# Kernel optimization log

Hardware: AMD Instinct MI355X
Metric: run time of the kernel (lower is better)

## Reference

```python
import jax, jax.numpy as jnp
import numpy as np

MARGIN = 0.3
NEG_FILL = 1000000.0


def setup_inputs() -> dict:
    key = jax.random.key(0)
    k1, k2 = jax.random.split(key)
    features = jax.random.normal(k1, (8192, 128), dtype=jnp.float32)
    labels = jax.random.randint(k2, (8192,), 0, 512, dtype=jnp.int64)
    return {"features": features, "labels": labels}


def _triplet_loss(features, labels):
    N = features.shape[0]
    # pairwise euclidean distances via gram trick (matches torch.cdist p=2)
    sq = jnp.sum(features * features, axis=1)               # [N]
    d2 = sq[:, None] + sq[None, :] - 2.0 * (features @ features.T)
    d2 = jnp.maximum(d2, 0.0)
    # guard sqrt(0) on diagonal for clean gradients
    dist = jnp.where(d2 > 0.0, jnp.sqrt(jnp.where(d2 > 0.0, d2, 1.0)), 0.0)  # [N,N]

    same = labels[:, None] == labels[None, :]
    eye = jnp.eye(N, dtype=bool)
    is_pos = same & ~eye
    is_neg = ~same

    neg_inf = jnp.float32(-jnp.inf)
    pos_inf = jnp.float32(jnp.inf)
    has_pos = jnp.any(is_pos, axis=1)
    has_neg = jnp.any(is_neg, axis=1)
    # hardest positive: masked row max; empty -> 0.0
    dist_ap = jnp.max(jnp.where(is_pos, dist, neg_inf), axis=1)
    dist_ap = jnp.where(has_pos, dist_ap, 0.0)
    # hardest negative: masked row min; empty -> 1e6
    dist_an = jnp.min(jnp.where(is_neg, dist, pos_inf), axis=1)
    dist_an = jnp.where(has_neg, dist_an, NEG_FILL)

    # MarginRankingLoss with y=1: mean(max(0, margin - (dist_an - dist_ap)))
    return jnp.mean(jnp.maximum(0.0, MARGIN - (dist_an - dist_ap)))


def reference(features, labels):
    return _triplet_loss(features, labels)
```

## Files before the change

### kernel.cpp

```cpp
#include <hip/hip_runtime.h>
#include <hip/hip_bf16.h>
#include <math.h>

#define N 8192
#define D 128
#define MARGIN_V 0.3f
#define NEG_FILL 1000000.0f

typedef short bf16x8 __attribute__((ext_vector_type(8)));
typedef float f32x4  __attribute__((ext_vector_type(4)));


__global__ __launch_bounds__(256) void convert_kernel(const float* __restrict__ F,
                                                      unsigned short* __restrict__ Fb,
                                                      float* __restrict__ sq,
                                                      unsigned* __restrict__ ap,
                                                      unsigned* __restrict__ an) {
    __shared__ float red[16][17];
    const int g   = blockIdx.x;
    const int tid = threadIdx.x;
    const int q = tid >> 6, L = tid & 63;
    const int m = L & 15, j8 = (L >> 4) * 8;

    const float* src = F + (size_t)(16 * g + m) * D + 32 * q + j8;
    float4 v0 = *(const float4*)src;
    float4 v1 = *(const float4*)(src + 4);

    float s = v0.x * v0.x + v0.y * v0.y + v0.z * v0.z + v0.w * v0.w
            + v1.x * v1.x + v1.y * v1.y + v1.z * v1.z + v1.w * v1.w;

    union { bf16x8 v; __hip_bfloat162 h2[4]; } pk;
    pk.h2[0] = __float22bfloat162_rn({v0.x, v0.y});
    pk.h2[1] = __float22bfloat162_rn({v0.z, v0.w});
    pk.h2[2] = __float22bfloat162_rn({v1.x, v1.y});
    pk.h2[3] = __float22bfloat162_rn({v1.z, v1.w});
    *(bf16x8*)&Fb[(size_t)g * 2048 + tid * 8] = pk.v;

    red[m][q * 4 + (L >> 4)] = s;
    __syncthreads();
    if (tid < 16) {
        float t = 0.f;
        #pragma unroll
        for (int c = 0; c < 16; ++c) t += red[tid][c];
        sq[16 * g + tid] = t;
    }
    int gid = blockIdx.x * 256 + tid;
    if (gid < N) { ap[gid] = 0u; an[gid] = 0x7F800000u; }
}

__global__ __launch_bounds__(256, 2) void gemm_kernel(const unsigned short* __restrict__ Fb,
                                                      const float* __restrict__ sq,
                                                      const int* __restrict__ lab,
                                                      unsigned* __restrict__ ap,
                                                      unsigned* __restrict__ an) {
    const int tid  = threadIdx.x;
    const int wave = tid >> 6, lane = tid & 63;
    const int quad = lane >> 4, lr = lane & 15;
    const int S = blockIdx.x >> 4;
    const int C = blockIdx.x & 15;
    const int R0   = S * 256 + wave * 64;
    const int g0   = R0 >> 4;
    const int cg0  = C * 32;
    const int colb = C * 512;

    bf16x8 af[4][4];
    #pragma unroll
    for (int a = 0; a < 4; ++a)
        #pragma unroll
        for (int ks = 0; ks < 4; ++ks) {
            af[a][ks] = *(const bf16x8*)&Fb[(((size_t)(g0 + a) * 4 + ks) * 64 + lane) * 8];
            unsigned* uw = (unsigned*)&af[a][ks];
            #pragma unroll
            for (int w = 0; w < 4; ++w)
                uw[w] = (uw[w] + 0x00800080u) ^ 0x80008000u;
        }

    int4 labi4[4];
    #pragma unroll
    for (int a = 0; a < 4; ++a)
        labi4[a] = *(const int4*)&lab[R0 + a * 16 + quad * 4];

    float rowP[4][4], rowN[4][4];
    #pragma unroll
    for (int a = 0; a < 4; ++a)
        #pragma unroll
        for (int r = 0; r < 4; ++r) { rowP[a][r] = -INFINITY; rowN[a][r] = INFINITY; }

#define LOADT(T, BF, SQJ, LABJ)                                                   \
    {                                                                             \
        _Pragma("unroll")                                                         \
        for (int b = 0; b < 2; ++b) {                                             \
            int gb = cg0 + 2 * (T) + b;                                           \
            _Pragma("unroll")                                                     \
            for (int ks = 0; ks < 4; ++ks)                                        \
                BF[b][ks] = *(const bf16x8*)&Fb[(((size_t)gb * 4 + ks) * 64 + lane) * 8]; \
            SQJ[b]  = sq[colb + (T) * 32 + b * 16 + lr];                          \
            LABJ[b] = lab[colb + (T) * 32 + b * 16 + lr];                         \
        }                                                                         \
    }

#define COMP(BF, SQJ, LABJ)                                                       \
    {                                                                             \
        f32x4 acc[4][2];                                                          \
        _Pragma("unroll")                                                         \
        for (int a = 0; a < 4; ++a)                                               \
            _Pragma("unroll")                                                     \
            for (int b = 0; b < 2; ++b)                                           \
                acc[a][b] = {SQJ[b], SQJ[b], SQJ[b], SQJ[b]};                     \
        _Pragma("unroll")                                                         \
        for (int ks = 0; ks < 4; ++ks)                                            \
            _Pragma("unroll")                                                     \
            for (int a = 0; a < 4; ++a)                                           \
                _Pragma("unroll")                                                 \
                for (int b = 0; b < 2; ++b)                                       \
                    acc[a][b] = __builtin_amdgcn_mfma_f32_16x16x32_bf16(          \
                        af[a][ks], BF[b][ks], acc[a][b], 0, 0, 0);                \
        _Pragma("unroll")                                                         \
        for (int a = 0; a < 4; ++a)                                               \
            _Pragma("unroll")                                                     \
            for (int r = 0; r < 4; ++r) {                                         \
                float u0 = acc[a][0][r], u1 = acc[a][1][r];                       \
                bool s0 = (labi4[a][r] == LABJ[0]);                               \
                bool s1 = (labi4[a][r] == LABJ[1]);                               \
                float p0 = s0 ? u0 : -INFINITY;                                   \
                float p1 = s1 ? u1 : -INFINITY;                                   \
                float n0 = s0 ? INFINITY : u0;                                    \
                float n1 = s1 ? INFINITY : u1;                                    \
                rowP[a][r] = fmaxf(fmaxf(rowP[a][r], p0), p1);                    \
                rowN[a][r] = fminf(fminf(rowN[a][r], n0), n1);                    \
            }                                                                     \
    }

    bf16x8 b0[2][4], b1[2][4];
    float sq0[2], sq1[2];
    int   lb0[2], lb1[2];
    LOADT(0, b0, sq0, lb0);
    #pragma unroll 1
    for (int t = 0; t < 16; t += 2) {
        LOADT(t + 1, b1, sq1, lb1);
        COMP(b0, sq0, lb0);
        if (t + 2 < 16) LOADT(t + 2, b0, sq0, lb0);
        COMP(b1, sq1, lb1);
    }
#undef LOADT
#undef COMP

    #pragma unroll
    for (int a = 0; a < 4; ++a)
        #pragma unroll
        for (int r = 0; r < 4; ++r) {
            float p = rowP[a][r], n = rowN[a][r];
            #pragma unroll
            for (int off = 1; off < 16; off <<= 1) {
                p = fmaxf(p, __shfl_xor(p, off));
                n = fminf(n, __shfl_xor(n, off));
            }
            rowP[a][r] = p; rowN[a][r] = n;
        }
    if (lr == 0) {
        #pragma unroll
        for (int a = 0; a < 4; ++a) {
            f32x4 sqi4 = *(const f32x4*)&sq[R0 + a * 16 + quad * 4];
            #pragma unroll
            for (int r = 0; r < 4; ++r) {
                int row = R0 + a * 16 + quad * 4 + r;
                float pd2 = fmaxf(sqi4[r] + rowP[a][r], 0.f);
                float nd2 = fmaxf(sqi4[r] + rowN[a][r], 0.f);
                atomicMax(&ap[row], __float_as_uint(pd2));
                atomicMin(&an[row], __float_as_uint(nd2));
            }
        }
    }
}

__global__ __launch_bounds__(256) void loss_kernel(const float* __restrict__ ap,
                                                   const float* __restrict__ an,
                                                   float* __restrict__ out) {
    int tid = threadIdx.x;
    float sum = 0.f;
    #pragma unroll
    for (int k = 0; k < 8; ++k) {
        int i = k * 1024 + tid * 4;
        f32x4 a4 = *(const f32x4*)&ap[i];
        f32x4 n4 = *(const f32x4*)&an[i];
        #pragma unroll
        for (int c = 0; c < 4; ++c) {
            float apd = __builtin_amdgcn_sqrtf(a4[c]);
            float anv = n4[c];
            float and_ = (anv < INFINITY) ? __builtin_amdgcn_sqrtf(anv) : NEG_FILL;
            sum += fmaxf(0.f, MARGIN_V - (and_ - apd));
        }
    }
    #pragma unroll
    for (int off = 32; off >= 1; off >>= 1) sum += __shfl_xor(sum, off);
    __shared__ float s4[4];
    if ((tid & 63) == 0) s4[tid >> 6] = sum;
    __syncthreads();
    if (tid == 0) out[0] = (s4[0] + s4[1] + s4[2] + s4[3]) * (1.0f / (float)N);
}

extern "C" void kernel_launch(void* const* d_in, const int* in_sizes, int n_in,
                              void* d_out, int out_size, void* d_ws, size_t ws_size,
                              hipStream_t stream) {
    const float* F   = (const float*)d_in[0];
    const int*   lab = (const int*)d_in[1];

    unsigned short* Fb = (unsigned short*)d_ws;
    float*          sq = (float*)(Fb + (size_t)N * D);
    unsigned*       ap = (unsigned*)(sq + N);
    unsigned*       an = ap + N;

    convert_kernel<<<N / 16, 256, 0, stream>>>(F, Fb, sq, ap, an);
    gemm_kernel<<<512, 256, 0, stream>>>(Fb, sq, lab, ap, an);
    loss_kernel<<<1, 256, 0, stream>>>((const float*)ap, (const float*)an, (float*)d_out);
}
```

Measured before the change: 85.46 us.

## Stage B tiles into shared LDS via global_load_lds with double buffering

Each block now copies the column-side bf16 tiles from global memory into a double-buffered LDS buffer using global_load_lds, and all four waves read fragments from LDS. Previously every wave loaded the same tiles into its own registers. The aim is to cut redundant global/L2 traffic for the B operand by a factor of the wave count. The cost is two block-wide barriers per iteration. The barrier placed right after issuing the next tile's load may force a wait on that load before compute, which would serialize load and MFMA work that the old register prefetch overlapped.

```diff
diff --git a/kernel.cpp b/kernel.cpp
--- a/kernel.cpp
+++ b/kernel.cpp
@@ -9,6 +9,9 @@
 
 typedef short bf16x8 __attribute__((ext_vector_type(8)));
 typedef float f32x4  __attribute__((ext_vector_type(4)));
+
+typedef __attribute__((address_space(1))) const unsigned short g_us;
+typedef __attribute__((address_space(3))) unsigned short l_us;
 
 
 __global__ __launch_bounds__(256) void convert_kernel(const float* __restrict__ F,
@@ -53,6 +56,7 @@
                                                       const int* __restrict__ lab,
                                                       unsigned* __restrict__ ap,
                                                       unsigned* __restrict__ an) {
+    __shared__ unsigned short Bs[2][4096];
     const int tid  = threadIdx.x;
     const int wave = tid >> 6, lane = tid & 63;
     const int quad = lane >> 4, lr = lane & 15;
@@ -86,21 +90,33 @@
         #pragma unroll
         for (int r = 0; r < 4; ++r) { rowP[a][r] = -INFINITY; rowN[a][r] = INFINITY; }
 
-#define LOADT(T, BF, SQJ, LABJ)                                                   \
+#define STAGE(T, P)                                                               \
     {                                                                             \
+        const unsigned short* gs = Fb + (size_t)(cg0 + 2 * (T)) * 2048;           \
+        _Pragma("unroll")                                                         \
+        for (int i = 0; i < 2; ++i)                                               \
+            __builtin_amdgcn_global_load_lds(                                     \
+                (g_us*)(gs + i * 2048 + wave * 512 + lane * 8),                   \
+                (l_us*)&Bs[P][i * 2048 + wave * 512], 16, 0, 0);                  \
+    }
+
+#define LOADSL(T, SQ, LB)                                                         \
+    {                                                                             \
         _Pragma("unroll")                                                         \
         for (int b = 0; b < 2; ++b) {                                             \
-            int gb = cg0 + 2 * (T) + b;                                           \
+            SQ[b] = sq[colb + (T) * 32 + b * 16 + lr];                            \
+            LB[b] = lab[colb + (T) * 32 + b * 16 + lr];                           \
+        }                                                                         \
+    }
+
+#define COMP(P, SQJ, LABJ)                                                        \
+    {                                                                             \
+        bf16x8 bfr[2][4];                                                         \
+        _Pragma("unroll")                                                         \
+        for (int b = 0; b < 2; ++b)                                               \
             _Pragma("unroll")                                                     \
             for (int ks = 0; ks < 4; ++ks)                                        \
-                BF[b][ks] = *(const bf16x8*)&Fb[(((size_t)gb * 4 + ks) * 64 + lane) * 8]; \
-            SQJ[b]  = sq[colb + (T) * 32 + b * 16 + lr];                          \
-            LABJ[b] = lab[colb + (T) * 32 + b * 16 + lr];                         \
-        }                                                                         \
-    }
-
-#define COMP(BF, SQJ, LABJ)                                                       \
-    {                                                                             \
+                bfr[b][ks] = *(const bf16x8*)&Bs[P][b * 2048 + ks * 512 + lane * 8]; \
         f32x4 acc[4][2];                                                          \
         _Pragma("unroll")                                                         \
         for (int a = 0; a < 4; ++a)                                               \
@@ -114,7 +130,7 @@
                 _Pragma("unroll")                                                 \
                 for (int b = 0; b < 2; ++b)                                       \
                     acc[a][b] = __builtin_amdgcn_mfma_f32_16x16x32_bf16(          \
-                        af[a][ks], BF[b][ks], acc[a][b], 0, 0, 0);                \
+                        af[a][ks], bfr[b][ks], acc[a][b], 0, 0, 0);               \
         _Pragma("unroll")                                                         \
         for (int a = 0; a < 4; ++a)                                               \
             _Pragma("unroll")                                                     \
@@ -131,18 +147,26 @@
             }                                                                     \
     }
 
-    bf16x8 b0[2][4], b1[2][4];
-    float sq0[2], sq1[2];
-    int   lb0[2], lb1[2];
-    LOADT(0, b0, sq0, lb0);
+    float sqc[2], sqn[2];
+    int   lbc[2], lbn[2];
+    STAGE(0, 0);
+    LOADSL(0, sqc, lbc);
     #pragma unroll 1
-    for (int t = 0; t < 16; t += 2) {
-        LOADT(t + 1, b1, sq1, lb1);
-        COMP(b0, sq0, lb0);
-        if (t + 2 < 16) LOADT(t + 2, b0, sq0, lb0);
-        COMP(b1, sq1, lb1);
-    }
-#undef LOADT
+    for (int t = 0; t < 16; ++t) {
+        __syncthreads();
+        if (t + 1 < 16) {
+            STAGE(t + 1, (t + 1) & 1);
+            LOADSL(t + 1, sqn, lbn);
+        }
+        __syncthreads();
+        COMP(t & 1, sqc, lbc);
+        if (t + 1 < 16) {
+            sqc[0] = sqn[0]; sqc[1] = sqn[1];
+            lbc[0] = lbn[0]; lbc[1] = lbn[1];
+        }
+    }
+#undef STAGE
+#undef LOADSL
 #undef COMP
 
     #pragma unroll
```

New measurement: 84.89 us. No clear change (-0.7%).
